# Kernel tuning notes

Hardware: AMD Instinct MI355X
Metric: run time of the kernel (lower is better)

## Reference

```python
import jax, jax.numpy as jnp
import numpy as np

B = 8192
IN = 2048
H = 2048


def setup_inputs() -> dict:
    key = jax.random.key(0)
    ks = jax.random.split(key, 16)
    s_in = 1.0 / np.sqrt(IN)
    s_h = 1.0 / np.sqrt(H)
    inp = {
        "x": jax.random.normal(ks[0], (B, IN), jnp.float32),
        "h": jax.random.normal(ks[1], (B, H), jnp.float32),
        "c": jax.random.normal(ks[2], (B, H), jnp.float32),
        # Linear weights stored torch-style as [out, in]
        "w_xf": jax.random.uniform(ks[3], (H, IN), jnp.float32, -s_in, s_in),
        "w_hf": jax.random.uniform(ks[4], (H, H), jnp.float32, -s_h, s_h),
        "b_f": jax.random.normal(ks[5], (H,), jnp.float32),
        "w_xi": jax.random.uniform(ks[6], (H, IN), jnp.float32, -s_in, s_in),
        "w_hi": jax.random.uniform(ks[7], (H, H), jnp.float32, -s_h, s_h),
        "b_i": jax.random.normal(ks[8], (H,), jnp.float32),
        "w_xo": jax.random.uniform(ks[9], (H, IN), jnp.float32, -s_in, s_in),
        "w_ho": jax.random.uniform(ks[10], (H, H), jnp.float32, -s_h, s_h),
        "b_o": jax.random.normal(ks[11], (H,), jnp.float32),
        "w_xc": jax.random.uniform(ks[12], (H, IN), jnp.float32, -s_in, s_in),
        "w_hc": jax.random.uniform(ks[13], (H, H), jnp.float32, -s_h, s_h),
        "b_c": jax.random.normal(ks[14], (H,), jnp.float32),
    }
    return inp


def reference(x, h, c, w_xf, w_hf, b_f, w_xi, w_hi, b_i,
              w_xo, w_ho, b_o, w_xc, w_hc, b_c):
    # Fuse the 8 small GEMMs into 2 batched GEMMs (x-side, h-side).
    Wx = jnp.concatenate([w_xf, w_xi, w_xo, w_xc], axis=0)  # [4H, IN]
    Wh = jnp.concatenate([w_hf, w_hi, w_ho, w_hc], axis=0)  # [4H, H]
    b = jnp.concatenate([b_f, b_i, b_o, b_c], axis=0)       # [4H]
    gates = x @ Wx.T + h @ Wh.T + b                          # [B, 4H]
    hd = h.shape[-1]
    f = jax.nn.sigmoid(gates[:, 0 * hd:1 * hd])
    i = jax.nn.sigmoid(gates[:, 1 * hd:2 * hd])
    o = jax.nn.sigmoid(gates[:, 2 * hd:3 * hd])
    c_tilde = jnp.tanh(gates[:, 3 * hd:4 * hd])
    c_new = f * c + i * c_tilde
    h_new = o * jnp.tanh(c_new)
    return (h_new, c_new)
```

## Files before the change

### kernel.cpp

```cpp
#include <hip/hip_runtime.h>


typedef __attribute__((ext_vector_type(8))) short short8;
typedef __attribute__((ext_vector_type(8))) __bf16 bf16x8;
typedef __attribute__((ext_vector_type(16))) float f32x16;

#define GLDS(gp, lp)                                                        \
  __builtin_amdgcn_global_load_lds(                                         \
      (const __attribute__((address_space(1))) void*)(gp),                  \
      (__attribute__((address_space(3))) void*)(lp), 16, 0, 0)

__device__ __forceinline__ unsigned short f2bf(float f) {
  unsigned u = __builtin_bit_cast(unsigned, f);
  u = (u + 0x7FFFu + ((u >> 16) & 1u)) >> 16;
  return (unsigned short)u;
}

__global__ void pack_x_kernel(const float* __restrict__ x,
                              const float* __restrict__ h,
                              short* __restrict__ X2) {
  long tid = (long)blockIdx.x * blockDim.x + threadIdx.x;
  long flat = tid * 8;
  int row = (int)(flat >> 12);
  int k = (int)(flat & 4095);
  const float* src = (k < 2048) ? (x + (long)row * 2048 + k)
                                : (h + (long)row * 2048 + (k - 2048));
  float4 a = *(const float4*)src;
  float4 b = *(const float4*)(src + 4);
  short8 o;
  o[0] = (short)f2bf(a.x); o[1] = (short)f2bf(a.y);
  o[2] = (short)f2bf(a.z); o[3] = (short)f2bf(a.w);
  o[4] = (short)f2bf(b.x); o[5] = (short)f2bf(b.y);
  o[6] = (short)f2bf(b.z); o[7] = (short)f2bf(b.w);
  *(short8*)(X2 + flat) = o;
}

__global__ void pack_w_kernel(const float* __restrict__ wxf, const float* __restrict__ wxi,
                              const float* __restrict__ wxo, const float* __restrict__ wxc,
                              const float* __restrict__ whf, const float* __restrict__ whi,
                              const float* __restrict__ who, const float* __restrict__ whc,
                              short* __restrict__ W3) {
  long tid = (long)blockIdx.x * blockDim.x + threadIdx.x;
  long flat = tid * 8;
  int j = (int)(flat >> 12);
  int k = (int)(flat & 4095);
  int hc = ((j >> 6) << 4) | (j & 15);
  int g = (j >> 4) & 3;
  const float* base;
  if (k < 2048) {
    const float* wx = (g == 0) ? wxf : (g == 1) ? wxi : (g == 2) ? wxo : wxc;
    base = wx + (long)hc * 2048 + k;
  } else {
    const float* wh = (g == 0) ? whf : (g == 1) ? whi : (g == 2) ? who : whc;
    base = wh + (long)hc * 2048 + (k - 2048);
  }
  float4 a = *(const float4*)base;
  float4 b = *(const float4*)(base + 4);
  short8 o;
  o[0] = (short)f2bf(a.x); o[1] = (short)f2bf(a.y);
  o[2] = (short)f2bf(a.z); o[3] = (short)f2bf(a.w);
  o[4] = (short)f2bf(b.x); o[5] = (short)f2bf(b.y);
  o[6] = (short)f2bf(b.z); o[7] = (short)f2bf(b.w);
  *(short8*)(W3 + flat) = o;
}

__global__ __launch_bounds__(512, 2) void lstm_fused_gemm(
    const short* __restrict__ X2, const short* __restrict__ W3,
    const float* __restrict__ cin,
    const float* __restrict__ bF, const float* __restrict__ bI,
    const float* __restrict__ bO, const float* __restrict__ bC,
    float* __restrict__ hout, float* __restrict__ cout_) {
  __shared__ __align__(16) short lds[65536];

  const int tid = threadIdx.x;
  const int lane = tid & 63;
  const int w = tid >> 6;
  const int wm = w >> 2;
  const int wn = w & 3;

  const int bid = blockIdx.x;
  const int bM = (bid & 7) * 4 + ((bid >> 3) & 3);
  const int bN = bid >> 5;

  const int sPair = tid >> 3;
  const int sSlog = (tid & 7) ^ (sPair & 7);
  const int srow = sPair * 2 + (sSlog >> 2);
  const int skoff = (sSlog & 3) * 8;
  const short* aRow0 = X2 + ((size_t)(bM * 256 + srow)) * 4096 + skoff;
  const short* aRow1 = aRow0 + (size_t)128 * 4096;
  const short* bRow0 = W3 + ((size_t)(bN * 256 + srow)) * 4096 + skoff;
  const short* bRow1 = bRow0 + (size_t)128 * 4096;

#define STAGEQ(q, tt, bb) do {                                               \
    const int _kh = (q) >> 1;                                                \
    const short* _g0; const short* _g1;                                      \
    if (((q) & 1) == 0) {                                                    \
      _g0 = aRow0 + (tt) * 64 + _kh * 32;                                    \
      _g1 = aRow1 + (tt) * 64 + _kh * 32;                                    \
    } else {                                                                 \
      _g0 = bRow0 + (tt) * 64 + _kh * 32;                                    \
      _g1 = bRow1 + (tt) * 64 + _kh * 32;                                    \
    }                                                                        \
    char* _l0 = (char*)lds + (bb) * 65536 + (q) * 16384 + tid * 16;          \
    GLDS(_g0, _l0);                                                          \
    GLDS(_g1, _l0 + 8192);                                                   \
  } while (0)

  const int l31 = lane & 31, hi2 = lane >> 5;
  const int rA = wm * 128 + l31;
  const int pA = rA >> 1;
  const int aoffE = pA * 128 + ((((rA & 1) * 4) + 0 + hi2) ^ (pA & 7)) * 16;
  const int aoffO = pA * 128 + ((((rA & 1) * 4) + 2 + hi2) ^ (pA & 7)) * 16;
  const int rB = wn * 64 + l31;
  const int pB = rB >> 1;
  const int boffE = 16384 + pB * 128 + ((((rB & 1) * 4) + 0 + hi2) ^ (pB & 7)) * 16;
  const int boffO = 16384 + pB * 128 + ((((rB & 1) * 4) + 2 + hi2) ^ (pB & 7)) * 16;

#define LDSRD(off) (*(const bf16x8*)((const char*)lds + (off)))
#define MFMA32(a, b, c) __builtin_amdgcn_mfma_f32_32x32x16_bf16((a), (b), (c), 0, 0, 0)

  f32x16 acc[4][2] = {};

  STAGEQ(0, 0, 0); STAGEQ(1, 0, 0); STAGEQ(2, 0, 0); STAGEQ(3, 0, 0);
  asm volatile("s_waitcnt vmcnt(0)" ::: "memory");
  __builtin_amdgcn_s_barrier();

#pragma unroll 2
  for (int t = 0; t < 64; ++t) {
    const int cur = t & 1, nxt = cur ^ 1;
    const int bo = cur << 16;
    const int t1 = (t + 1) & 63;
    bf16x8 a[4], b[2];

#pragma unroll
    for (int m = 0; m < 4; ++m) a[m] = LDSRD(bo + aoffE + m * 2048);
#pragma unroll
    for (int n = 0; n < 2; ++n) b[n] = LDSRD(bo + boffE + n * 2048);
    STAGEQ(0, t1, nxt);
    __builtin_amdgcn_s_barrier();
    __builtin_amdgcn_s_setprio(1);
#pragma unroll
    for (int n = 0; n < 2; ++n)
#pragma unroll
      for (int m = 0; m < 4; ++m) acc[m][n] = MFMA32(a[m], b[n], acc[m][n]);
    __builtin_amdgcn_s_setprio(0);

#pragma unroll
    for (int m = 0; m < 4; ++m) a[m] = LDSRD(bo + aoffO + m * 2048);
#pragma unroll
    for (int n = 0; n < 2; ++n) b[n] = LDSRD(bo + boffO + n * 2048);
    STAGEQ(1, t1, nxt);
    asm volatile("s_waitcnt vmcnt(4)" ::: "memory");
    __builtin_amdgcn_s_barrier();
    __builtin_amdgcn_s_setprio(1);
#pragma unroll
    for (int n = 0; n < 2; ++n)
#pragma unroll
      for (int m = 0; m < 4; ++m) acc[m][n] = MFMA32(a[m], b[n], acc[m][n]);
    __builtin_amdgcn_s_setprio(0);

#pragma unroll
    for (int m = 0; m < 4; ++m) a[m] = LDSRD(bo + 32768 + aoffE + m * 2048);
#pragma unroll
    for (int n = 0; n < 2; ++n) b[n] = LDSRD(bo + 32768 + boffE + n * 2048);
    STAGEQ(2, t1, nxt);
    __builtin_amdgcn_s_barrier();
    __builtin_amdgcn_s_setprio(1);
#pragma unroll
    for (int n = 0; n < 2; ++n)
#pragma unroll
      for (int m = 0; m < 4; ++m) acc[m][n] = MFMA32(a[m], b[n], acc[m][n]);
    __builtin_amdgcn_s_setprio(0);

#pragma unroll
    for (int m = 0; m < 4; ++m) a[m] = LDSRD(bo + 32768 + aoffO + m * 2048);
#pragma unroll
    for (int n = 0; n < 2; ++n) b[n] = LDSRD(bo + 32768 + boffO + n * 2048);
    STAGEQ(3, t1, nxt);
    asm volatile("s_waitcnt vmcnt(4)" ::: "memory");
    __builtin_amdgcn_s_barrier();
    __builtin_amdgcn_s_setprio(1);
#pragma unroll
    for (int n = 0; n < 2; ++n)
#pragma unroll
      for (int m = 0; m < 4; ++m) acc[m][n] = MFMA32(a[m], b[n], acc[m][n]);
    __builtin_amdgcn_s_setprio(0);
  }

  const int l15 = lane & 15;
  const int bit4 = (lane >> 4) & 1;
  const int hc = (bN * 4 + wn) * 16 + l15;
  const float vbF = bF[hc], vbI = bI[hc], vbO = bO[hc], vbC = bC[hc];
  float* const cPtr = cout_;
#pragma unroll
  for (int m = 0; m < 4; ++m) {
    const int rowbase = bM * 256 + wm * 128 + m * 32 + 4 * hi2;
#pragma unroll
    for (int r = 0; r < 16; ++r) {
      const int rowg = rowbase + (r & 3) + 8 * (r >> 2);
      const float a0 = acc[m][0][r];
      const float a1 = acc[m][1][r];
      const float s0 = __shfl_xor(a0, 16);
      const float s1 = __shfl_xor(a1, 16);
      const float gf = (bit4 ? s0 : a0) + vbF;
      const float gi = (bit4 ? a0 : s0) + vbI;
      const float go = (bit4 ? s1 : a1) + vbO;
      const float gc = (bit4 ? a1 : s1) + vbC;
      const float fg = 1.f / (1.f + __expf(-gf));
      const float ig = 1.f / (1.f + __expf(-gi));
      const float og = 1.f / (1.f + __expf(-go));
      const float ct = 2.f / (1.f + __expf(-2.f * gc)) - 1.f;
      const size_t idx = (size_t)rowg * 2048 + hc;
      const float cn = fg * cin[idx] + ig * ct;
      const float hn = og * (2.f / (1.f + __expf(-2.f * cn)) - 1.f);
      float* dst = bit4 ? cPtr : hout;
      dst[idx] = bit4 ? cn : hn;
    }
  }
}

extern "C" void kernel_launch(void* const* d_in, const int* in_sizes, int n_in,
                              void* d_out, int out_size, void* d_ws, size_t ws_size,
                              hipStream_t stream) {
  const float* x    = (const float*)d_in[0];
  const float* h    = (const float*)d_in[1];
  const float* c    = (const float*)d_in[2];
  const float* w_xf = (const float*)d_in[3];
  const float* w_hf = (const float*)d_in[4];
  const float* b_f  = (const float*)d_in[5];
  const float* w_xi = (const float*)d_in[6];
  const float* w_hi = (const float*)d_in[7];
  const float* b_i  = (const float*)d_in[8];
  const float* w_xo = (const float*)d_in[9];
  const float* w_ho = (const float*)d_in[10];
  const float* b_o  = (const float*)d_in[11];
  const float* w_xc = (const float*)d_in[12];
  const float* w_hc = (const float*)d_in[13];
  const float* b_c  = (const float*)d_in[14];

  float* hout  = (float*)d_out;
  float* cout_ = hout + (size_t)8192 * 2048;

  short* X2 = (short*)d_ws;
  short* W3 = X2 + (size_t)8192 * 4096;

  const int packBlocks = (int)(((long)8192 * 4096 / 8) / 256);
  pack_x_kernel<<<packBlocks, 256, 0, stream>>>(x, h, X2);
  pack_w_kernel<<<packBlocks, 256, 0, stream>>>(w_xf, w_xi, w_xo, w_xc,
                                                w_hf, w_hi, w_ho, w_hc, W3);

  lstm_fused_gemm<<<1024, 512, 0, stream>>>(X2, W3, c, b_f, b_i, b_o, b_c,
                                            hout, cout_);
}
```

Measured before the change: 637.3 us.

## Shrink GEMM tile to 256x128 with triple-buffered LDS pipeline

The fused LSTM GEMM block tile goes from 256x256 with 8 waves to 256x128 with 4 waves, launching 2048 blocks instead of 1024. The K step per stage drops to 32, and LDS is split into three rotating 24KB buffers, so loads run two stages ahead with a single barrier per iteration instead of four. This is meant to cut barrier overhead, hide global-load latency better, and improve occupancy or tail balance. The cost is lower arithmetic intensity per block, since more A-tile reloads are needed, plus more loop iterations.

```diff
diff --git a/kernel.cpp b/kernel.cpp
--- a/kernel.cpp
+++ b/kernel.cpp
@@ -64,19 +64,19 @@
   *(short8*)(W3 + flat) = o;
 }
 
-__global__ __launch_bounds__(512, 2) void lstm_fused_gemm(
+__global__ __launch_bounds__(256, 2) void lstm_fused_gemm(
     const short* __restrict__ X2, const short* __restrict__ W3,
     const float* __restrict__ cin,
     const float* __restrict__ bF, const float* __restrict__ bI,
     const float* __restrict__ bO, const float* __restrict__ bC,
     float* __restrict__ hout, float* __restrict__ cout_) {
-  __shared__ __align__(16) short lds[65536];
+  __shared__ __align__(16) short lds[36864];
 
   const int tid = threadIdx.x;
   const int lane = tid & 63;
   const int w = tid >> 6;
-  const int wm = w >> 2;
-  const int wn = w & 3;
+  const int wm = w >> 1;
+  const int wn = w & 1;
 
   const int bid = blockIdx.x;
   const int bM = (bid & 7) * 4 + ((bid >> 3) & 3);
@@ -84,112 +84,82 @@
 
   const int sPair = tid >> 3;
   const int sSlog = (tid & 7) ^ (sPair & 7);
-  const int srow = sPair * 2 + (sSlog >> 2);
-  const int skoff = (sSlog & 3) * 8;
-  const short* aRow0 = X2 + ((size_t)(bM * 256 + srow)) * 4096 + skoff;
-  const short* aRow1 = aRow0 + (size_t)128 * 4096;
-  const short* bRow0 = W3 + ((size_t)(bN * 256 + srow)) * 4096 + skoff;
-  const short* bRow1 = bRow0 + (size_t)128 * 4096;
-
-#define STAGEQ(q, tt, bb) do {                                               \
-    const int _kh = (q) >> 1;                                                \
-    const short* _g0; const short* _g1;                                      \
-    if (((q) & 1) == 0) {                                                    \
-      _g0 = aRow0 + (tt) * 64 + _kh * 32;                                    \
-      _g1 = aRow1 + (tt) * 64 + _kh * 32;                                    \
-    } else {                                                                 \
-      _g0 = bRow0 + (tt) * 64 + _kh * 32;                                    \
-      _g1 = bRow1 + (tt) * 64 + _kh * 32;                                    \
-    }                                                                        \
-    char* _l0 = (char*)lds + (bb) * 65536 + (q) * 16384 + tid * 16;          \
-    GLDS(_g0, _l0);                                                          \
-    GLDS(_g1, _l0 + 8192);                                                   \
+  const int srow  = sPair * 2 + (sSlog >> 2);
+  const int sks   = ((sSlog & 1) << 1) | ((sSlog >> 1) & 1);
+  const short* aS = X2 + ((size_t)(bM * 256 + srow)) * 4096 + sks * 8;
+  const short* bS = W3 + ((size_t)(bN * 128 + srow)) * 4096 + sks * 8;
+
+#define STAGE_A(ts, bb) do {                                                 \
+    GLDS(aS + (ts) * 32,                 (char*)lds + (bb) + tid * 16);      \
+    GLDS(aS + 64 * 4096 + (ts) * 32,     (char*)lds + (bb) + tid * 16 + 4096); \
+    GLDS(aS + 128 * 4096 + (ts) * 32,    (char*)lds + (bb) + tid * 16 + 8192); \
+    GLDS(aS + 192 * 4096 + (ts) * 32,    (char*)lds + (bb) + tid * 16 + 12288); \
+  } while (0)
+#define STAGE_B(ts, bb) do {                                                 \
+    GLDS(bS + (ts) * 32,              (char*)lds + (bb) + 16384 + tid * 16); \
+    GLDS(bS + 64 * 4096 + (ts) * 32,  (char*)lds + (bb) + 16384 + tid * 16 + 4096); \
   } while (0)
 
   const int l31 = lane & 31, hi2 = lane >> 5;
   const int rA = wm * 128 + l31;
   const int pA = rA >> 1;
-  const int aoffE = pA * 128 + ((((rA & 1) * 4) + 0 + hi2) ^ (pA & 7)) * 16;
-  const int aoffO = pA * 128 + ((((rA & 1) * 4) + 2 + hi2) ^ (pA & 7)) * 16;
+  const int eA = (rA & 1) * 4 + hi2 * 2;
+  const int aoffE = pA * 128 + ((eA ^ (pA & 7))) * 16;
+  const int aoffO = pA * 128 + (((eA + 1) ^ (pA & 7))) * 16;
   const int rB = wn * 64 + l31;
   const int pB = rB >> 1;
-  const int boffE = 16384 + pB * 128 + ((((rB & 1) * 4) + 0 + hi2) ^ (pB & 7)) * 16;
-  const int boffO = 16384 + pB * 128 + ((((rB & 1) * 4) + 2 + hi2) ^ (pB & 7)) * 16;
+  const int eB = (rB & 1) * 4 + hi2 * 2;
+  const int boffE = 16384 + pB * 128 + ((eB ^ (pB & 7))) * 16;
+  const int boffO = 16384 + pB * 128 + (((eB + 1) ^ (pB & 7))) * 16;
 
 #define LDSRD(off) (*(const bf16x8*)((const char*)lds + (off)))
 #define MFMA32(a, b, c) __builtin_amdgcn_mfma_f32_32x32x16_bf16((a), (b), (c), 0, 0, 0)
 
   f32x16 acc[4][2] = {};
 
-  STAGEQ(0, 0, 0); STAGEQ(1, 0, 0); STAGEQ(2, 0, 0); STAGEQ(3, 0, 0);
-  asm volatile("s_waitcnt vmcnt(0)" ::: "memory");
+  STAGE_A(0, 0);     STAGE_B(0, 0);
+  STAGE_A(1, 24576); STAGE_B(1, 24576);
+  asm volatile("s_waitcnt vmcnt(6)" ::: "memory");
   __builtin_amdgcn_s_barrier();
 
-#pragma unroll 2
-  for (int t = 0; t < 64; ++t) {
-    const int cur = t & 1, nxt = cur ^ 1;
-    const int bo = cur << 16;
-    const int t1 = (t + 1) & 63;
-    bf16x8 a[4], b[2];
-
-#pragma unroll
-    for (int m = 0; m < 4; ++m) a[m] = LDSRD(bo + aoffE + m * 2048);
-#pragma unroll
-    for (int n = 0; n < 2; ++n) b[n] = LDSRD(bo + boffE + n * 2048);
-    STAGEQ(0, t1, nxt);
+  int bufA = 0, bufB = 24576, bufC = 49152;
+
+  for (int t = 0; t < 128; ++t) {
+    const int ts = (t + 2) & 127;
+    bf16x8 aE[4], aO[4], bE[2], bO[2];
+
+#pragma unroll
+    for (int m = 0; m < 4; ++m) aE[m] = LDSRD(bufA + aoffE + m * 2048);
+#pragma unroll
+    for (int n = 0; n < 2; ++n) bE[n] = LDSRD(bufA + boffE + n * 2048);
+#pragma unroll
+    for (int m = 0; m < 4; ++m) aO[m] = LDSRD(bufA + aoffO + m * 2048);
+#pragma unroll
+    for (int n = 0; n < 2; ++n) bO[n] = LDSRD(bufA + boffO + n * 2048);
+
+    STAGE_A(ts, bufC);
+    STAGE_B(ts, bufC);
+
+    __builtin_amdgcn_s_setprio(1);
+#pragma unroll
+    for (int n = 0; n < 2; ++n)
+#pragma unroll
+      for (int m = 0; m < 4; ++m) acc[m][n] = MFMA32(aE[m], bE[n], acc[m][n]);
+#pragma unroll
+    for (int n = 0; n < 2; ++n)
+#pragma unroll
+      for (int m = 0; m < 4; ++m) acc[m][n] = MFMA32(aO[m], bO[n], acc[m][n]);
+    __builtin_amdgcn_s_setprio(0);
+
+    asm volatile("s_waitcnt vmcnt(6)" ::: "memory");
     __builtin_amdgcn_s_barrier();
-    __builtin_amdgcn_s_setprio(1);
-#pragma unroll
-    for (int n = 0; n < 2; ++n)
-#pragma unroll
-      for (int m = 0; m < 4; ++m) acc[m][n] = MFMA32(a[m], b[n], acc[m][n]);
-    __builtin_amdgcn_s_setprio(0);
-
-#pragma unroll
-    for (int m = 0; m < 4; ++m) a[m] = LDSRD(bo + aoffO + m * 2048);
-#pragma unroll
-    for (int n = 0; n < 2; ++n) b[n] = LDSRD(bo + boffO + n * 2048);
-    STAGEQ(1, t1, nxt);
-    asm volatile("s_waitcnt vmcnt(4)" ::: "memory");
-    __builtin_amdgcn_s_barrier();
-    __builtin_amdgcn_s_setprio(1);
-#pragma unroll
-    for (int n = 0; n < 2; ++n)
-#pragma unroll
-      for (int m = 0; m < 4; ++m) acc[m][n] = MFMA32(a[m], b[n], acc[m][n]);
-    __builtin_amdgcn_s_setprio(0);
-
-#pragma unroll
-    for (int m = 0; m < 4; ++m) a[m] = LDSRD(bo + 32768 + aoffE + m * 2048);
-#pragma unroll
-    for (int n = 0; n < 2; ++n) b[n] = LDSRD(bo + 32768 + boffE + n * 2048);
-    STAGEQ(2, t1, nxt);
-    __builtin_amdgcn_s_barrier();
-    __builtin_amdgcn_s_setprio(1);
-#pragma unroll
-    for (int n = 0; n < 2; ++n)
-#pragma unroll
-      for (int m = 0; m < 4; ++m) acc[m][n] = MFMA32(a[m], b[n], acc[m][n]);
-    __builtin_amdgcn_s_setprio(0);
-
-#pragma unroll
-    for (int m = 0; m < 4; ++m) a[m] = LDSRD(bo + 32768 + aoffO + m * 2048);
-#pragma unroll
-    for (int n = 0; n < 2; ++n) b[n] = LDSRD(bo + 32768 + boffO + n * 2048);
-    STAGEQ(3, t1, nxt);
-    asm volatile("s_waitcnt vmcnt(4)" ::: "memory");
-    __builtin_amdgcn_s_barrier();
-    __builtin_amdgcn_s_setprio(1);
-#pragma unroll
-    for (int n = 0; n < 2; ++n)
-#pragma unroll
-      for (int m = 0; m < 4; ++m) acc[m][n] = MFMA32(a[m], b[n], acc[m][n]);
-    __builtin_amdgcn_s_setprio(0);
+
+    const int tmp = bufA; bufA = bufB; bufB = bufC; bufC = tmp;
   }
 
   const int l15 = lane & 15;
   const int bit4 = (lane >> 4) & 1;
-  const int hc = (bN * 4 + wn) * 16 + l15;
+  const int hc = (bN * 2 + wn) * 16 + l15;
   const float vbF = bF[hc], vbI = bI[hc], vbO = bO[hc], vbC = bC[hc];
   float* const cPtr = cout_;
 #pragma unroll
@@ -249,6 +219,6 @@
   pack_w_kernel<<<packBlocks, 256, 0, stream>>>(w_xf, w_xi, w_xo, w_xc,
                                                 w_hf, w_hi, w_ho, w_hc, W3);
 
-  lstm_fused_gemm<<<1024, 512, 0, stream>>>(X2, W3, c, b_f, b_i, b_o, b_c,
+  lstm_fused_gemm<<<2048, 256, 0, stream>>>(X2, W3, c, b_f, b_i, b_o, b_c,
                                             hout, cout_);
 }
```

New measurement: 664.5 us. +4.3%, slower.

## Switch LDS tiles to per-wave 64-byte row swizzle and front-load staging

Applied to the files above, without the earlier changes.

Staging now gives each wave its own contiguous LDS block for global_load_lds. The shared-memory layout changes from paired 128-byte rows with an 8-way XOR swizzle to 64-byte rows with a 4-way XOR swizzle, and the fragment read offsets are updated to match. Prefetch of the next K tile is rescheduled: three of the four quarters are issued in the first compute phase and the last in the second, instead of one quarter per phase, and the vmcnt waits are adjusted. The aim is cheaper address generation, fewer LDS bank conflicts and earlier prefetch. The risks are a less effective swizzle and looser wait-count ordering.

```diff
diff --git a/kernel.cpp b/kernel.cpp
--- a/kernel.cpp
+++ b/kernel.cpp
@@ -82,46 +82,46 @@
   const int bM = (bid & 7) * 4 + ((bid >> 3) & 3);
   const int bN = bid >> 5;
 
-  const int sPair = tid >> 3;
-  const int sSlog = (tid & 7) ^ (sPair & 7);
-  const int srow = sPair * 2 + (sSlog >> 2);
-  const int skoff = (sSlog & 3) * 8;
-  const short* aRow0 = X2 + ((size_t)(bM * 256 + srow)) * 4096 + skoff;
+  const int ci = w * 64 + lane;
+  const int r0 = ci >> 2;
+  const int ss = (ci & 3) ^ ((r0 >> 1) & 3);
+  const short* aRow0 = X2 + ((size_t)(bM * 256 + r0)) * 4096 + ss * 8;
   const short* aRow1 = aRow0 + (size_t)128 * 4096;
-  const short* bRow0 = W3 + ((size_t)(bN * 256 + srow)) * 4096 + skoff;
+  const short* bRow0 = W3 + ((size_t)(bN * 256 + r0)) * 4096 + ss * 8;
   const short* bRow1 = bRow0 + (size_t)128 * 4096;
-
-#define STAGEQ(q, tt, bb) do {                                               \
+  const int wOff = w * 1024;
+
+#define STAGE2(q, tt, bb) do {                                               \
     const int _kh = (q) >> 1;                                                \
     const short* _g0; const short* _g1;                                      \
-    if (((q) & 1) == 0) {                                                    \
+    if ((q) == 0 || (q) == 2) {                                              \
       _g0 = aRow0 + (tt) * 64 + _kh * 32;                                    \
       _g1 = aRow1 + (tt) * 64 + _kh * 32;                                    \
     } else {                                                                 \
       _g0 = bRow0 + (tt) * 64 + _kh * 32;                                    \
       _g1 = bRow1 + (tt) * 64 + _kh * 32;                                    \
     }                                                                        \
-    char* _l0 = (char*)lds + (bb) * 65536 + (q) * 16384 + tid * 16;          \
+    char* _l0 = (char*)lds + (bb) * 65536 + (q) * 16384 + wOff;              \
     GLDS(_g0, _l0);                                                          \
     GLDS(_g1, _l0 + 8192);                                                   \
   } while (0)
 
   const int l31 = lane & 31, hi2 = lane >> 5;
   const int rA = wm * 128 + l31;
-  const int pA = rA >> 1;
-  const int aoffE = pA * 128 + ((((rA & 1) * 4) + 0 + hi2) ^ (pA & 7)) * 16;
-  const int aoffO = pA * 128 + ((((rA & 1) * 4) + 2 + hi2) ^ (pA & 7)) * 16;
+  const int fA = (rA >> 1) & 3;
+  const int aoffE = rA * 64 + ((0 + hi2) ^ fA) * 16;
+  const int aoffO = rA * 64 + ((2 + hi2) ^ fA) * 16;
   const int rB = wn * 64 + l31;
-  const int pB = rB >> 1;
-  const int boffE = 16384 + pB * 128 + ((((rB & 1) * 4) + 0 + hi2) ^ (pB & 7)) * 16;
-  const int boffO = 16384 + pB * 128 + ((((rB & 1) * 4) + 2 + hi2) ^ (pB & 7)) * 16;
+  const int fB = (rB >> 1) & 3;
+  const int boffE = 16384 + rB * 64 + ((0 + hi2) ^ fB) * 16;
+  const int boffO = 16384 + rB * 64 + ((2 + hi2) ^ fB) * 16;
 
 #define LDSRD(off) (*(const bf16x8*)((const char*)lds + (off)))
 #define MFMA32(a, b, c) __builtin_amdgcn_mfma_f32_32x32x16_bf16((a), (b), (c), 0, 0, 0)
 
   f32x16 acc[4][2] = {};
 
-  STAGEQ(0, 0, 0); STAGEQ(1, 0, 0); STAGEQ(2, 0, 0); STAGEQ(3, 0, 0);
+  STAGE2(0, 0, 0); STAGE2(1, 0, 0); STAGE2(3, 0, 0); STAGE2(2, 0, 0);
   asm volatile("s_waitcnt vmcnt(0)" ::: "memory");
   __builtin_amdgcn_s_barrier();
 
@@ -136,7 +136,9 @@
     for (int m = 0; m < 4; ++m) a[m] = LDSRD(bo + aoffE + m * 2048);
 #pragma unroll
     for (int n = 0; n < 2; ++n) b[n] = LDSRD(bo + boffE + n * 2048);
-    STAGEQ(0, t1, nxt);
+    STAGE2(0, t1, nxt);
+    STAGE2(1, t1, nxt);
+    STAGE2(3, t1, nxt);
     __builtin_amdgcn_s_barrier();
     __builtin_amdgcn_s_setprio(1);
 #pragma unroll
@@ -149,8 +151,8 @@
     for (int m = 0; m < 4; ++m) a[m] = LDSRD(bo + aoffO + m * 2048);
 #pragma unroll
     for (int n = 0; n < 2; ++n) b[n] = LDSRD(bo + boffO + n * 2048);
-    STAGEQ(1, t1, nxt);
-    asm volatile("s_waitcnt vmcnt(4)" ::: "memory");
+    STAGE2(2, t1, nxt);
+    asm volatile("s_waitcnt vmcnt(8)" ::: "memory");
     __builtin_amdgcn_s_barrier();
     __builtin_amdgcn_s_setprio(1);
 #pragma unroll
@@ -163,7 +165,6 @@
     for (int m = 0; m < 4; ++m) a[m] = LDSRD(bo + 32768 + aoffE + m * 2048);
 #pragma unroll
     for (int n = 0; n < 2; ++n) b[n] = LDSRD(bo + 32768 + boffE + n * 2048);
-    STAGEQ(2, t1, nxt);
     __builtin_amdgcn_s_barrier();
     __builtin_amdgcn_s_setprio(1);
 #pragma unroll
@@ -176,7 +177,6 @@
     for (int m = 0; m < 4; ++m) a[m] = LDSRD(bo + 32768 + aoffO + m * 2048);
 #pragma unroll
     for (int n = 0; n < 2; ++n) b[n] = LDSRD(bo + 32768 + boffO + n * 2048);
-    STAGEQ(3, t1, nxt);
     asm volatile("s_waitcnt vmcnt(4)" ::: "memory");
     __builtin_amdgcn_s_barrier();
     __builtin_amdgcn_s_setprio(1);
```

Result: no change. 640.7 us (+0.5%).
